# Performance work log

Measured on AMD Instinct MI355X. Metric: run time of the kernel, lower is better.

The kernel has to match this reference:

```python
import jax, jax.numpy as jnp
import numpy as np

HIDDEN = 1024
HEADS = 16
HEAD_DIM = HIDDEN // HEADS


def setup_inputs() -> dict:
    key = jax.random.key(0)
    ks = jax.random.split(key, 8)
    B, S = 2, 2048
    scale = 1.0 / np.sqrt(HIDDEN)
    inp = {
        "hidden_states": jax.random.normal(ks[0], (B, S, HIDDEN), dtype=jnp.float32),
        "attention_mask": jnp.zeros((B, 1, 1, S), dtype=jnp.float32),
        "q_w": jax.random.normal(ks[1], (HIDDEN, HIDDEN), dtype=jnp.float32) * scale,
        "q_b": jnp.zeros((HIDDEN,), dtype=jnp.float32),
        "k_w": jax.random.normal(ks[2], (HIDDEN, HIDDEN), dtype=jnp.float32) * scale,
        "k_b": jnp.zeros((HIDDEN,), dtype=jnp.float32),
        "v_w": jax.random.normal(ks[3], (HIDDEN, HIDDEN), dtype=jnp.float32) * scale,
        "v_b": jnp.zeros((HIDDEN,), dtype=jnp.float32),
    }
    return inp


def _split_heads(x):
    # [B, S, H] -> [B, heads, S, head_dim]
    B, S, _ = x.shape
    return x.reshape(B, S, HEADS, HEAD_DIM).transpose(0, 2, 1, 3)


def reference(hidden_states, attention_mask, q_w, q_b, k_w, k_b, v_w, v_b):
    # Linear projections (torch Linear: x @ W.T + b; here weights stored as [in, out])
    q = _split_heads(hidden_states @ q_w + q_b)  # [B, h, S, d]
    k = _split_heads(hidden_states @ k_w + k_b)
    v = _split_heads(hidden_states @ v_w + v_b)

    scores = jnp.einsum("bhqd,bhkd->bhqk", q, k) / jnp.sqrt(jnp.float32(HEAD_DIM))
    scores = scores + attention_mask  # additive mask, broadcast [B,1,1,S]
    probs = jax.nn.softmax(scores, axis=-1)
    # dropout prob = 0.0 -> identity
    ctx = jnp.einsum("bhqk,bhkd->bhqd", probs, v)  # [B, h, S, d]
    B, _, S, _ = ctx.shape
    ctx = ctx.transpose(0, 2, 1, 3).reshape(B, S, HIDDEN)
    return ctx
```

## Files before the change

kernel.cpp:

```cpp
#include <hip/hip_runtime.h>

typedef __bf16 bf16;
typedef __attribute__((ext_vector_type(8))) __bf16 bf16x8;
typedef __attribute__((ext_vector_type(4))) __bf16 bf16x4;
typedef __attribute__((ext_vector_type(4))) float f32x4;

#define MFMA(a, b, c) __builtin_amdgcn_mfma_f32_16x16x32_bf16((a), (b), (c), 0, 0, 0)
#define LOG2E 1.44269504088896340736f

__device__ __forceinline__ bf16x8 cvt8(float4 a, float4 b) {
  bf16x8 r;
  r[0] = (bf16)a.x; r[1] = (bf16)a.y; r[2] = (bf16)a.z; r[3] = (bf16)a.w;
  r[4] = (bf16)b.x; r[5] = (bf16)b.y; r[6] = (bf16)b.z; r[7] = (bf16)b.w;
  return r;
}

__device__ __forceinline__ void stage16(const bf16* g, bf16* l) {
  __builtin_amdgcn_global_load_lds(
      (const __attribute__((address_space(1))) void*)g,
      (__attribute__((address_space(3))) void*)l, 16, 0, 0);
}

__global__ __launch_bounds__(256)
void cvt(const float* __restrict__ hs, const float* __restrict__ qw,
         const float* __restrict__ kw, const float* __restrict__ vw,
         bf16* __restrict__ Xb, bf16* __restrict__ Wt) {
  const int bid = blockIdx.x, tid = threadIdx.x;
  if (bid < 2048) {
    size_t off = (size_t)bid * 2048 + tid * 8;
    float4 x0 = *(const float4*)(hs + off);
    float4 x1 = *(const float4*)(hs + off + 4);
    *(bf16x8*)(Xb + off) = cvt8(x0, x1);
  } else {
    int t = bid - 2048;
    int z = t >> 8, ti = t & 255;
    const float* W = (z == 0) ? qw : (z == 1) ? kw : vw;
    int k0 = (ti >> 4) * 64, n0 = (ti & 15) * 64;
    __shared__ bf16 T[64 * 72];
    #pragma unroll
    for (int i = 0; i < 16; ++i) {
      int e = i * 256 + tid;
      int kr = e >> 6, nc = e & 63;
      T[nc * 72 + kr] = (bf16)W[(size_t)(k0 + kr) * 1024 + n0 + nc];
    }
    __syncthreads();
    #pragma unroll
    for (int i = 0; i < 2; ++i) {
      int e = i * 256 + tid;
      int nr = e >> 3, kg = e & 7;
      *(bf16x8*)(Wt + (size_t)z * 1048576 + (size_t)(n0 + nr) * 1024 + k0 + kg * 8) =
          *(const bf16x8*)&T[nr * 72 + kg * 8];
    }
  }
}

__global__ __launch_bounds__(256, 3)
void qkv_gemm(const bf16* __restrict__ Xb, const bf16* __restrict__ Wt,
              const float* __restrict__ qbias, const float* __restrict__ kbias,
              const float* __restrict__ vbias,
              bf16* __restrict__ qo, bf16* __restrict__ ko, bf16* __restrict__ vo) {
  const int blk = blockIdx.x;
  const int xcd = blk & 7, slot = blk >> 3;
  const int mb = xcd * 4 + slot / 24;
  const int nb = slot % 24;
  const int z = nb >> 3, nbm = nb & 7;
  const bf16* W = Wt + (size_t)z * 1048576;

  const int tid = threadIdx.x;
  const int wave = tid >> 6, lane = tid & 63, quad = lane >> 4, c = lane & 15;
  const int wr = wave >> 1, wc = wave & 1;
  const int r4 = lane >> 2;
  const int g4 = (lane & 3) ^ (r4 & 3);

  __shared__ bf16 As[128 * 32];
  __shared__ bf16 Bs[128 * 32];

  const bf16* aS0 = Xb + (size_t)(mb * 128 + wave * 16 + r4) * 1024 + g4 * 8;
  const bf16* aS1 = aS0 + (size_t)64 * 1024;
  const bf16* bS0 = W + (size_t)(nbm * 128 + wave * 16 + r4) * 1024 + g4 * 8;
  const bf16* bS1 = bS0 + (size_t)64 * 1024;
  bf16* aD0 = &As[(wave * 16) * 32];
  bf16* aD1 = &As[(64 + wave * 16) * 32];
  bf16* bD0 = &Bs[(wave * 16) * 32];
  bf16* bD1 = &Bs[(64 + wave * 16) * 32];

  int aOff[4], bOff[4];
  #pragma unroll
  for (int t = 0; t < 4; ++t) {
    aOff[t] = (wr * 64 + t * 16 + c) * 32 + ((quad ^ (c & 3)) << 3);
    bOff[t] = (wc * 64 + t * 16 + c) * 32 + ((quad ^ (c & 3)) << 3);
  }

  f32x4 acc[4][4] = {};

  for (int k0 = 0; k0 < 1024; k0 += 32) {
    stage16(aS0 + k0, aD0);
    stage16(aS1 + k0, aD1);
    stage16(bS0 + k0, bD0);
    stage16(bS1 + k0, bD1);
    __syncthreads();
    bf16x8 af[4];
    #pragma unroll
    for (int rt = 0; rt < 4; ++rt) af[rt] = *(const bf16x8*)&As[aOff[rt]];
    #pragma unroll
    for (int nt = 0; nt < 4; ++nt) {
      bf16x8 bfrag = *(const bf16x8*)&Bs[bOff[nt]];
      #pragma unroll
      for (int rt = 0; rt < 4; ++rt)
        acc[rt][nt] = MFMA(af[rt], bfrag, acc[rt][nt]);
    }
    __syncthreads();
  }

  const float* bias = (z == 0) ? qbias : (z == 1) ? kbias : vbias;
  float bv[4];
  #pragma unroll
  for (int nt = 0; nt < 4; ++nt)
    bv[nt] = bias[nbm * 128 + wc * 64 + nt * 16 + c];

  if (z == 2) {
    #pragma unroll
    for (int rt = 0; rt < 4; ++rt)
      #pragma unroll
      for (int nt = 0; nt < 4; ++nt) {
        int m0 = mb * 128 + wr * 64 + rt * 16 + 4 * quad;
        int n = nbm * 128 + wc * 64 + nt * 16 + c;
        bf16x4 pk;
        #pragma unroll
        for (int reg = 0; reg < 4; ++reg) pk[reg] = (bf16)(acc[rt][nt][reg] + bv[nt]);
        int b = m0 >> 11, s0 = m0 & 2047, h = n >> 6, d = n & 63;
        *(bf16x4*)&vo[(((size_t)b * 16 + h) * 64 + d) * 2048 + s0] = pk;
      }
  } else {
    bf16* dst = (z == 0) ? qo : ko;
    const float scale = (z == 0) ? 0.125f * LOG2E : 1.0f;
    #pragma unroll
    for (int rt = 0; rt < 4; ++rt)
      #pragma unroll
      for (int nt = 0; nt < 4; ++nt)
        #pragma unroll
        for (int reg = 0; reg < 4; ++reg) {
          float v = (acc[rt][nt][reg] + bv[nt]) * scale;
          int m = mb * 128 + wr * 64 + rt * 16 + 4 * quad + reg;
          int n = nbm * 128 + wc * 64 + nt * 16 + c;
          int b = m >> 11, s = m & 2047, h = n >> 6, d = n & 63;
          dst[(((size_t)b * 16 + h) * 2048 + s) * 64 + d] = (bf16)v;
        }
  }
}

__global__ __launch_bounds__(256, 4)
void attn(const bf16* __restrict__ qg, const bf16* __restrict__ kg,
          const bf16* __restrict__ vtg, const float* __restrict__ mask,
          float* __restrict__ out) {
  const int blk = blockIdx.x;
  const int xcd = blk & 7, slot = blk >> 3;
  const int bh = xcd * 4 + (slot >> 5);
  const int qblk = slot & 31;
  const int b = bh >> 4, h = bh & 15;
  const int tid = threadIdx.x;
  const int wave = tid >> 6, lane = tid & 63, quad = lane >> 4, c = lane & 15;
  const int lrow = lane >> 3, lg = (lane & 7) ^ lrow;

  __shared__ bf16 Ks[64 * 64];
  __shared__ bf16 Vs[64 * 64];
  __shared__ bf16 Ps[4][1024];

  const bf16* qb_ = qg + (size_t)bh * 2048 * 64;
  const bf16* kb_ = kg + (size_t)bh * 2048 * 64;
  const bf16* vb_ = vtg + (size_t)bh * 64 * 2048;

  bf16x8 qf[2];
  #pragma unroll
  for (int ch = 0; ch < 2; ++ch)
    qf[ch] = *(const bf16x8*)(qb_ +
        (size_t)(qblk * 64 + wave * 16 + c) * 64 + ch * 32 + quad * 8);

  f32x4 o[4] = {};
  float lsum[4] = {};

  for (int kt = 0; kt < 32; ++kt) {
    #pragma unroll
    for (int i = 0; i < 2; ++i) {
      int r = wave * 16 + i * 8;
      stage16(kb_ + (size_t)(kt * 64 + r + lrow) * 64 + lg * 8, &Ks[r * 64]);
      stage16(vb_ + (size_t)(r + lrow) * 2048 + kt * 64 + lg * 8, &Vs[r * 64]);
    }
    __syncthreads();

    f32x4 s[4] = {};
    #pragma unroll
    for (int nt = 0; nt < 4; ++nt)
      #pragma unroll
      for (int ch = 0; ch < 2; ++ch) {
        bf16x8 kf = *(const bf16x8*)&Ks[(nt * 16 + c) * 64 +
                                        ((((ch << 2) | quad) ^ (c & 7)) << 3)];
        s[nt] = MFMA(qf[ch], kf, s[nt]);
      }

    float mv[4];
    #pragma unroll
    for (int nt = 0; nt < 4; ++nt)
      mv[nt] = mask[b * 2048 + kt * 64 + nt * 16 + c] * LOG2E;

    #pragma unroll
    for (int nt = 0; nt < 4; ++nt)
      #pragma unroll
      for (int reg = 0; reg < 4; ++reg) {
        float p = __builtin_amdgcn_exp2f(s[nt][reg] + mv[nt]);
        lsum[reg] += p;
        int r = 4 * quad + reg;
        int gk = nt * 2 + (c >> 3);
        Ps[wave][r * 64 + ((gk ^ (r & 7)) << 3) + (c & 7)] = (bf16)p;
      }
    __asm__ volatile("s_waitcnt lgkmcnt(0)" ::: "memory");

    #pragma unroll
    for (int ch = 0; ch < 2; ++ch) {
      bf16x8 pa = *(const bf16x8*)&Ps[wave][c * 64 +
                                           ((((ch << 2) | quad) ^ (c & 7)) << 3)];
      #pragma unroll
      for (int nt = 0; nt < 4; ++nt) {
        bf16x8 vf = *(const bf16x8*)&Vs[(nt * 16 + c) * 64 +
                                        ((((ch << 2) | quad) ^ (c & 7)) << 3)];
        o[nt] = MFMA(pa, vf, o[nt]);
      }
    }
    __syncthreads();
  }

  #pragma unroll
  for (int reg = 0; reg < 4; ++reg) {
    float l = lsum[reg];
    #pragma unroll
    for (int off = 1; off < 16; off <<= 1) l += __shfl_xor(l, off, 64);
    float inv = 1.0f / l;
    int srow = qblk * 64 + wave * 16 + 4 * quad + reg;
    #pragma unroll
    for (int nt = 0; nt < 4; ++nt)
      out[((size_t)b * 2048 + srow) * 1024 + h * 64 + nt * 16 + c] =
          o[nt][reg] * inv;
  }
}

extern "C" void kernel_launch(void* const* d_in, const int* in_sizes, int n_in,
                              void* d_out, int out_size, void* d_ws, size_t ws_size,
                              hipStream_t stream) {
  const float* hs   = (const float*)d_in[0];
  const float* mask = (const float*)d_in[1];
  const float* qw   = (const float*)d_in[2];
  const float* qb   = (const float*)d_in[3];
  const float* kw   = (const float*)d_in[4];
  const float* kb   = (const float*)d_in[5];
  const float* vw   = (const float*)d_in[6];
  const float* vb   = (const float*)d_in[7];
  float* out = (float*)d_out;

  bf16* Xb   = (bf16*)d_ws;
  bf16* Wt   = Xb + (size_t)4096 * 1024;
  bf16* q_ws = Wt + (size_t)3 * 1048576;
  bf16* k_ws = q_ws + (size_t)4096 * 1024;
  bf16* v_ws = k_ws + (size_t)4096 * 1024;

  cvt<<<dim3(2816), 256, 0, stream>>>(hs, qw, kw, vw, Xb, Wt);
  qkv_gemm<<<dim3(768), 256, 0, stream>>>(Xb, Wt, qb, kb, vb, q_ws, k_ws, v_ws);
  attn<<<dim3(1024), 256, 0, stream>>>(q_ws, k_ws, v_ws, mask, out);
}
```

Before: 180.4 us.

## Double attention query tile per block and transpose MFMA operand order

Each attention block now handles 128 query rows instead of 64, with every wave owning two 16-row tiles. Each staged K/V tile is therefore reused across twice as many queries, which halves the global K/V traffic and the number of blocks. The MFMA operands are swapped so that scores come out transposed. This allows vectorized float4 mask loads, packed bf16 stores of P, and float4 output stores, and cuts the row-sum shuffle reduction to two steps. In exchange the kernel uses more registers, occupancy is lowered to 2 blocks, and the grid drops to 512 blocks.

```diff
diff --git a/kernel.cpp b/kernel.cpp
--- a/kernel.cpp
+++ b/kernel.cpp
@@ -3,6 +3,7 @@
 typedef __bf16 bf16;
 typedef __attribute__((ext_vector_type(8))) __bf16 bf16x8;
 typedef __attribute__((ext_vector_type(4))) __bf16 bf16x4;
+typedef __attribute__((ext_vector_type(2))) __bf16 bf16x2;
 typedef __attribute__((ext_vector_type(4))) float f32x4;
 
 #define MFMA(a, b, c) __builtin_amdgcn_mfma_f32_16x16x32_bf16((a), (b), (c), 0, 0, 0)
@@ -13,6 +14,12 @@
   r[0] = (bf16)a.x; r[1] = (bf16)a.y; r[2] = (bf16)a.z; r[3] = (bf16)a.w;
   r[4] = (bf16)b.x; r[5] = (bf16)b.y; r[6] = (bf16)b.z; r[7] = (bf16)b.w;
   return r;
+}
+
+__device__ __forceinline__ int pk2(float x, float y) {
+  union { bf16x2 h; int i; } u;
+  u.h[0] = (bf16)x; u.h[1] = (bf16)y;
+  return u.i;
 }
 
 __device__ __forceinline__ void stage16(const bf16* g, bf16* l) {
@@ -149,14 +156,14 @@
   }
 }
 
-__global__ __launch_bounds__(256, 4)
+__global__ __launch_bounds__(256, 2)
 void attn(const bf16* __restrict__ qg, const bf16* __restrict__ kg,
           const bf16* __restrict__ vtg, const float* __restrict__ mask,
           float* __restrict__ out) {
   const int blk = blockIdx.x;
   const int xcd = blk & 7, slot = blk >> 3;
-  const int bh = xcd * 4 + (slot >> 5);
-  const int qblk = slot & 31;
+  const int bh = xcd * 4 + (slot >> 4);
+  const int qblk = slot & 15;
   const int b = bh >> 4, h = bh & 15;
   const int tid = threadIdx.x;
   const int wave = tid >> 6, lane = tid & 63, quad = lane >> 4, c = lane & 15;
@@ -164,20 +171,24 @@
 
   __shared__ bf16 Ks[64 * 64];
   __shared__ bf16 Vs[64 * 64];
-  __shared__ bf16 Ps[4][1024];
+  __shared__ bf16 Ps[128 * 64];
 
   const bf16* qb_ = qg + (size_t)bh * 2048 * 64;
   const bf16* kb_ = kg + (size_t)bh * 2048 * 64;
   const bf16* vb_ = vtg + (size_t)bh * 64 * 2048;
-
-  bf16x8 qf[2];
-  #pragma unroll
-  for (int ch = 0; ch < 2; ++ch)
-    qf[ch] = *(const bf16x8*)(qb_ +
-        (size_t)(qblk * 64 + wave * 16 + c) * 64 + ch * 32 + quad * 8);
-
-  f32x4 o[4] = {};
-  float lsum[4] = {};
+  const float* mk_ = mask + (size_t)b * 2048;
+
+  bf16x8 qf[2][2];
+  #pragma unroll
+  for (int rt = 0; rt < 2; ++rt)
+    #pragma unroll
+    for (int ch = 0; ch < 2; ++ch)
+      qf[rt][ch] = *(const bf16x8*)(qb_ +
+          (size_t)(qblk * 128 + wave * 32 + rt * 16 + c) * 64 + ch * 32 + quad * 8);
+
+  const int sw2 = (c & 7) << 1;
+  f32x4 o[2][4] = {};
+  float lsum[2] = {0.f, 0.f};
 
   for (int kt = 0; kt < 32; ++kt) {
     #pragma unroll
@@ -188,58 +199,68 @@
     }
     __syncthreads();
 
-    f32x4 s[4] = {};
+    f32x4 s[2][4] = {};
     #pragma unroll
     for (int nt = 0; nt < 4; ++nt)
       #pragma unroll
       for (int ch = 0; ch < 2; ++ch) {
         bf16x8 kf = *(const bf16x8*)&Ks[(nt * 16 + c) * 64 +
                                         ((((ch << 2) | quad) ^ (c & 7)) << 3)];
-        s[nt] = MFMA(qf[ch], kf, s[nt]);
-      }
-
-    float mv[4];
-    #pragma unroll
-    for (int nt = 0; nt < 4; ++nt)
-      mv[nt] = mask[b * 2048 + kt * 64 + nt * 16 + c] * LOG2E;
-
-    #pragma unroll
-    for (int nt = 0; nt < 4; ++nt)
-      #pragma unroll
-      for (int reg = 0; reg < 4; ++reg) {
-        float p = __builtin_amdgcn_exp2f(s[nt][reg] + mv[nt]);
-        lsum[reg] += p;
-        int r = 4 * quad + reg;
-        int gk = nt * 2 + (c >> 3);
-        Ps[wave][r * 64 + ((gk ^ (r & 7)) << 3) + (c & 7)] = (bf16)p;
+        #pragma unroll
+        for (int rt = 0; rt < 2; ++rt)
+          s[rt][nt] = MFMA(kf, qf[rt][ch], s[rt][nt]);
+      }
+
+    #pragma unroll
+    for (int rt = 0; rt < 2; ++rt)
+      #pragma unroll
+      for (int nt = 0; nt < 4; ++nt) {
+        float4 mv = *(const float4*)&mk_[kt * 64 + nt * 16 + 4 * quad];
+        float p0 = __builtin_amdgcn_exp2f(fmaf(mv.x, LOG2E, s[rt][nt][0]));
+        float p1 = __builtin_amdgcn_exp2f(fmaf(mv.y, LOG2E, s[rt][nt][1]));
+        float p2 = __builtin_amdgcn_exp2f(fmaf(mv.z, LOG2E, s[rt][nt][2]));
+        float p3 = __builtin_amdgcn_exp2f(fmaf(mv.w, LOG2E, s[rt][nt][3]));
+        lsum[rt] += (p0 + p1) + (p2 + p3);
+        int gp = (nt * 4 + quad) ^ sw2;
+        int2 w = {pk2(p0, p1), pk2(p2, p3)};
+        *(int2*)&Ps[(wave * 32 + rt * 16 + c) * 64 + gp * 4] = w;
       }
     __asm__ volatile("s_waitcnt lgkmcnt(0)" ::: "memory");
 
     #pragma unroll
     for (int ch = 0; ch < 2; ++ch) {
-      bf16x8 pa = *(const bf16x8*)&Ps[wave][c * 64 +
-                                           ((((ch << 2) | quad) ^ (c & 7)) << 3)];
+      bf16x8 pb[2];
+      #pragma unroll
+      for (int rt = 0; rt < 2; ++rt) {
+        int gp = (ch * 8 + 2 * quad) ^ sw2;
+        pb[rt] = *(const bf16x8*)&Ps[(wave * 32 + rt * 16 + c) * 64 + gp * 4];
+      }
       #pragma unroll
       for (int nt = 0; nt < 4; ++nt) {
         bf16x8 vf = *(const bf16x8*)&Vs[(nt * 16 + c) * 64 +
                                         ((((ch << 2) | quad) ^ (c & 7)) << 3)];
-        o[nt] = MFMA(pa, vf, o[nt]);
-      }
-    }
-    __syncthreads();
-  }
-
-  #pragma unroll
-  for (int reg = 0; reg < 4; ++reg) {
-    float l = lsum[reg];
-    #pragma unroll
-    for (int off = 1; off < 16; off <<= 1) l += __shfl_xor(l, off, 64);
+        #pragma unroll
+        for (int rt = 0; rt < 2; ++rt)
+          o[rt][nt] = MFMA(vf, pb[rt], o[rt][nt]);
+      }
+    }
+    __syncthreads();
+  }
+
+  #pragma unroll
+  for (int rt = 0; rt < 2; ++rt) {
+    float l = lsum[rt];
+    l += __shfl_xor(l, 16, 64);
+    l += __shfl_xor(l, 32, 64);
     float inv = 1.0f / l;
-    int srow = qblk * 64 + wave * 16 + 4 * quad + reg;
-    #pragma unroll
-    for (int nt = 0; nt < 4; ++nt)
-      out[((size_t)b * 2048 + srow) * 1024 + h * 64 + nt * 16 + c] =
-          o[nt][reg] * inv;
+    int q = qblk * 128 + wave * 32 + rt * 16 + c;
+    float* op = out + ((size_t)b * 2048 + q) * 1024 + h * 64;
+    #pragma unroll
+    for (int nt = 0; nt < 4; ++nt) {
+      float4 v = {o[rt][nt][0] * inv, o[rt][nt][1] * inv,
+                  o[rt][nt][2] * inv, o[rt][nt][3] * inv};
+      *(float4*)&op[nt * 16 + 4 * quad] = v;
+    }
   }
 }
 
@@ -264,5 +285,5 @@
 
   cvt<<<dim3(2816), 256, 0, stream>>>(hs, qw, kw, vw, Xb, Wt);
   qkv_gemm<<<dim3(768), 256, 0, stream>>>(Xb, Wt, qb, kb, vb, q_ws, k_ws, v_ws);
-  attn<<<dim3(1024), 256, 0, stream>>>(q_ws, k_ws, v_ws, mask, out);
-}
+  attn<<<dim3(512), 256, 0, stream>>>(q_ws, k_ws, v_ws, mask, out);
+}
```

New measurement: 205.7 us. 14.1% more time.
